# Kernel optimization log

Measured on AMD Instinct MI355X. Metric: run time of the kernel, lower is better.

## Reference

```python
import jax, jax.numpy as jnp
import numpy as np

EMBED_DIM = 1024
NUM_HEADS = 16
HEAD_DIM = EMBED_DIM // NUM_HEADS
EPS = 1e-6


def setup_inputs() -> dict:
    key = jax.random.key(0)
    ks = jax.random.split(key, 11)
    Lq, Lk, N = 4096, 4096, 4
    s = 1.0 / np.sqrt(EMBED_DIM)
    inp = {
        'q': jax.random.normal(ks[0], (Lq, N, EMBED_DIM), dtype=jnp.float32),
        'k': jax.random.normal(ks[1], (Lk, N, EMBED_DIM), dtype=jnp.float32),
        'v': jax.random.normal(ks[2], (Lk, N, EMBED_DIM), dtype=jnp.float32),
        'Wq': jax.random.normal(ks[3], (EMBED_DIM, EMBED_DIM), dtype=jnp.float32) * s,
        'bq': jax.random.normal(ks[4], (EMBED_DIM,), dtype=jnp.float32) * s,
        'Wk': jax.random.normal(ks[5], (EMBED_DIM, EMBED_DIM), dtype=jnp.float32) * s,
        'bk': jax.random.normal(ks[6], (EMBED_DIM,), dtype=jnp.float32) * s,
        'Wv': jax.random.normal(ks[7], (EMBED_DIM, EMBED_DIM), dtype=jnp.float32) * s,
        'bv': jax.random.normal(ks[8], (EMBED_DIM,), dtype=jnp.float32) * s,
        'Wo': jax.random.normal(ks[9], (EMBED_DIM, EMBED_DIM), dtype=jnp.float32) * s,
        'bo': jax.random.normal(ks[10], (EMBED_DIM,), dtype=jnp.float32) * s,
    }
    return inp


def _feature_map(x):
    # F.elu(x) + 1
    return jax.nn.elu(x) + 1.0


def reference(q, k, v, Wq, bq, Wk, bk, Wv, bv, Wo, bo):
    Lq, N, E = q.shape
    Lk = k.shape[0]
    # torch Linear: y = x @ W.T + b
    qp = q @ Wq.T + bq
    kp = k @ Wk.T + bk
    vp = v @ Wv.T + bv
    # (L, N, E) -> (N, H, L, D)
    qh = qp.reshape(Lq, N, NUM_HEADS, HEAD_DIM).transpose(1, 2, 0, 3)
    kh = kp.reshape(Lk, N, NUM_HEADS, HEAD_DIM).transpose(1, 2, 0, 3)
    vh = vp.reshape(Lk, N, NUM_HEADS, HEAD_DIM).transpose(1, 2, 0, 3)
    qf = _feature_map(qh)
    kf = _feature_map(kh)
    k_sum = kf.sum(axis=2)                               # (N, H, D)
    kv = jnp.einsum('nhld,nhle->nhde', kf, vh)            # (N, H, D, D)
    z = 1.0 / (jnp.einsum('nhld,nhd->nhl', qf, k_sum) + EPS)
    out = jnp.einsum('nhld,nhde->nhle', qf, kv) * z[..., None]
    out = out.transpose(2, 0, 1, 3).reshape(Lq, N, E)
    out = out @ Wo.T + bo
    return out
```

## Files before the change

kernel.cpp:

```cpp
#include <hip/hip_runtime.h>
#include <hip/hip_bf16.h>
#include <cstdint>


typedef __attribute__((ext_vector_type(8))) short bf16x8;
typedef __attribute__((ext_vector_type(4))) float f32x4;

#define L_SEQ 4096
#define NBATCH 4
#define EMB 1024
#define NHEADS 16
#define HDIM 64
#define MROWS (L_SEQ * NBATCH)
#define NHG (NBATCH * NHEADS)
#define LCHUNK 512
#define NCHUNK (L_SEQ / LCHUNK)

__device__ __forceinline__ unsigned short f2bf(float f) {
  union { float f; uint32_t u; } v; v.f = f;
  uint32_t u = v.u;
  u += 0x7fffu + ((u >> 16) & 1u);
  return (unsigned short)(u >> 16);
}
__device__ __forceinline__ float bf2f(unsigned short s) {
  union { uint32_t u; float f; } v; v.u = ((uint32_t)s) << 16;
  return v.f;
}
__device__ __forceinline__ uint32_t pkbf(float a, float b) {
  union { float f; uint32_t u; } ua, ub; ua.f = a; ub.f = b;
  return ((ua.u + 0x8000u) >> 16) | ((ub.u + 0x8000u) & 0xffff0000u);
}

__global__ __launch_bounds__(256) void convert_kernel(const float* __restrict__ src,
                                                      unsigned short* __restrict__ dst,
                                                      int n) {
  int i = (blockIdx.x * 256 + threadIdx.x) * 4;
  if (i + 4 <= n) {
    float4 f = *(const float4*)(src + i);
    uint2 p;
    p.x = pkbf(f.x, f.y);
    p.y = pkbf(f.z, f.w);
    *(uint2*)(dst + i) = p;
  }
}

__global__ __launch_bounds__(256) void convert_w4(const float* __restrict__ s0,
                                                  const float* __restrict__ s1,
                                                  const float* __restrict__ s2,
                                                  const float* __restrict__ s3,
                                                  unsigned short* __restrict__ d0,
                                                  unsigned short* __restrict__ d1,
                                                  unsigned short* __restrict__ d2,
                                                  unsigned short* __restrict__ d3,
                                                  int n) {
  const int w = blockIdx.y;
  const float* src = (w == 0) ? s0 : (w == 1) ? s1 : (w == 2) ? s2 : s3;
  unsigned short* dst = (w == 0) ? d0 : (w == 1) ? d1 : (w == 2) ? d2 : d3;
  int i = (blockIdx.x * 256 + threadIdx.x) * 4;
  if (i + 4 <= n) {
    float4 f = *(const float4*)(src + i);
    uint2 p;
    p.x = pkbf(f.x, f.y);
    p.y = pkbf(f.z, f.w);
    *(uint2*)(dst + i) = p;
  }
}


#define STAGE_H(MATB, RH, SLOT, KTN)                                            \
  do {                                                                          \
    _Pragma("unroll")                                                           \
    for (int r_ = 0; r_ < 2; r_++) {                                            \
      const long grow_ = ((MATB) ? bcol0 : arow0) + (RH) * 128 + r_ * 64 + srowt;\
      const unsigned short* gp_ =                                               \
          ((MATB) ? B : A) + grow_ * (long)K + (KTN) + skoff;                   \
      __builtin_amdgcn_global_load_lds(                                         \
          (const __attribute__((address_space(1))) void*)gp_,                   \
          (__attribute__((address_space(3))) void*)(smem + (MATB) * 65536 +     \
              (SLOT) * 16384 + r_ * 8192 + wid * 1024),                         \
          16, 0, 0);                                                            \
    }                                                                           \
  } while (0)

#define MFMA_Q(AF, BF, MFB, NFB)                                                \
  do {                                                                          \
    __builtin_amdgcn_s_setprio(1);                                              \
    _Pragma("unroll")                                                           \
    for (int mi_ = 0; mi_ < 4; mi_++)                                           \
      _Pragma("unroll")                                                         \
      for (int ni_ = 0; ni_ < 2; ni_++)                                         \
        _Pragma("unroll")                                                       \
        for (int ks_ = 0; ks_ < 2; ks_++)                                       \
          acc[(MFB) + mi_][(NFB) + ni_] =                                       \
              __builtin_amdgcn_mfma_f32_16x16x32_bf16(                          \
                  AF[mi_ * 2 + ks_], BF[ni_ * 2 + ks_],                         \
                  acc[(MFB) + mi_][(NFB) + ni_], 0, 0, 0);                      \
    __builtin_amdgcn_s_setprio(0);                                              \
  } while (0)

#define PH_SYNC                                                                 \
  __builtin_amdgcn_s_barrier();                                                 \
  asm volatile("s_waitcnt lgkmcnt(0)" ::: "memory");                            \
  __builtin_amdgcn_sched_barrier(0);

#define TILE_T(SA, K1, K2, S01, S23, VMODE)                                     \
  do {                                                                          \
    bf16x8 af0[8], af1[8], bf0[4], bf1[4];                                      \
             \
    _Pragma("unroll")                                                           \
    for (int mi_ = 0; mi_ < 4; mi_++)                                           \
      _Pragma("unroll")                                                         \
      for (int ks_ = 0; ks_ < 2; ks_++)                                         \
        af0[mi_ * 2 + ks_] = *(const bf16x8*)(smem + ((SA) + wr) * 16384 + aRB +\
                                              mi_ * 2048 + akt[ks_]);           \
    _Pragma("unroll")                                                           \
    for (int ni_ = 0; ni_ < 2; ni_++)                                           \
      _Pragma("unroll")                                                         \
      for (int ks_ = 0; ks_ < 2; ks_++)                                         \
        bf0[ni_ * 2 + ks_] = *(const bf16x8*)(smem + 65536 +                    \
                                              ((SA) + (wc >> 1)) * 16384 + bRB +\
                                              ni_ * 2048 + akt[ks_]);           \
    if (S01) STAGE_H(0, 1, (SA) ^ 3, K1);                                       \
    PH_SYNC                                                                     \
    MFMA_Q(af0, bf0, 0, 0);                                                     \
    __builtin_amdgcn_s_barrier();                                               \
                                      \
    _Pragma("unroll")                                                           \
    for (int ni_ = 0; ni_ < 2; ni_++)                                           \
      _Pragma("unroll")                                                         \
      for (int ks_ = 0; ks_ < 2; ks_++)                                         \
        bf1[ni_ * 2 + ks_] = *(const bf16x8*)(smem + 65536 +                    \
                                              ((SA) + (wc >> 1)) * 16384 + bRB +\
                                              (ni_ + 2) * 2048 + akt[ks_]);     \
    if (S01) STAGE_H(1, 1, (SA) ^ 3, K1);                                       \
    PH_SYNC                                                                     \
    MFMA_Q(af0, bf1, 0, 2);                                                     \
    __builtin_amdgcn_s_barrier();                                               \
                                  \
    _Pragma("unroll")                                                           \
    for (int mi_ = 0; mi_ < 4; mi_++)                                           \
      _Pragma("unroll")                                                         \
      for (int ks_ = 0; ks_ < 2; ks_++)                                         \
        af1[mi_ * 2 + ks_] = *(const bf16x8*)(smem + ((SA) + wr) * 16384 + aRB +\
                                              (mi_ + 4) * 2048 + akt[ks_]);     \
    if (S23) STAGE_H(1, 0, (SA), K2);                                           \
    PH_SYNC                                                                     \
    MFMA_Q(af1, bf1, 4, 2);                                                     \
    __builtin_amdgcn_s_barrier();                                               \
                     \
    if (S23) STAGE_H(0, 0, (SA), K2);                                           \
    PH_SYNC                                                                     \
    MFMA_Q(af1, bf0, 4, 0);                                                     \
    if ((VMODE) == 1) asm volatile("s_waitcnt vmcnt(4)" ::: "memory");          \
    if ((VMODE) == 2) asm volatile("s_waitcnt vmcnt(0)" ::: "memory");          \
    __builtin_amdgcn_s_barrier();                                               \
  } while (0)

template <int MODE>
__global__ __launch_bounds__(512, 2) void gemm_bt(const unsigned short* __restrict__ A,
                                                  const unsigned short* __restrict__ B,
                                                  const float* __restrict__ bias,
                                                  void* __restrict__ Cout,
                                                  int M, int Nn, int K) {
  __shared__ __align__(16) char smem[131072];

  const int tid   = threadIdx.x;
  const int wid   = tid >> 6;
  const int lane  = tid & 63;
  const int col16 = lane & 15;
  const int quad  = lane >> 4;
  const int wr = wid >> 2;
  const int wc = wid & 3;
  const long arow0 = (long)blockIdx.x * 256;
  const long bcol0 = (long)blockIdx.y * 256;

  const int axor = (col16 & 7) << 4;
  int akt[2];
  akt[0] = (quad * 16) ^ axor;
  akt[1] = (64 + quad * 16) ^ axor;
  const int aRB = col16 * 128;
  const int bRB = ((wc & 1) * 64 + col16) * 128;

  const int srowt = tid >> 3;
  const int skoff = (((tid & 7) * 16) ^ ((srowt & 7) << 4)) >> 1;

  const int NT = K >> 6;

  STAGE_H(0, 0, 0, 0);
  STAGE_H(0, 1, 1, 0);
  STAGE_H(1, 0, 0, 0);
  STAGE_H(1, 1, 1, 0);
  STAGE_H(1, 0, 2, 64);
  STAGE_H(0, 0, 2, 64);

  const f32x4 fzero = {0.f, 0.f, 0.f, 0.f};
  f32x4 acc[8][4];
#pragma unroll
  for (int i = 0; i < 8; i++)
#pragma unroll
    for (int j = 0; j < 4; j++) acc[i][j] = fzero;

  asm volatile("s_waitcnt vmcnt(4)" ::: "memory");
  __builtin_amdgcn_s_barrier();

#pragma unroll 1
  for (int u = 0; u + 4 <= NT; u += 2) {
    TILE_T(0, (u + 1) * 64, (u + 2) * 64, 1, 1, 1);
    TILE_T(2, (u + 2) * 64, (u + 3) * 64, 1, 1, 1);
  }
  TILE_T(0, (NT - 1) * 64, 0, 1, 0, 2);
  TILE_T(2, 0, 0, 0, 0, 0);

  float bcol[4];
#pragma unroll
  for (int nf = 0; nf < 4; nf++) bcol[nf] = bias[bcol0 + wc * 64 + nf * 16 + col16];

  const int erow = tid >> 4;
  const int ecc  = tid & 15;

  if (MODE != 2) {
    unsigned short* epi = (unsigned short*)smem;
    const int EST = 264;
#pragma unroll
    for (int s = 0; s < 8; s++) {
      if ((s >> 2) == wr) {
        const int mfb = (s & 3) * 2;
#pragma unroll
        for (int ml = 0; ml < 2; ml++)
#pragma unroll
          for (int nf = 0; nf < 4; nf++)
#pragma unroll
            for (int rr = 0; rr < 4; rr++) {
              float vv = acc[mfb + ml][nf][rr] + bcol[nf];
              if (MODE == 0) vv = (vv > 0.f) ? (vv + 1.f) : __expf(vv);
              epi[(ml * 16 + quad * 4 + rr) * EST + wc * 64 + nf * 16 + col16] =
                  f2bf(vv);
            }
      }
      __syncthreads();
      {
        const long gr = arow0 + s * 32 + erow;
        const unsigned short* srcp = &epi[erow * EST + ecc * 16];
        uint4 a  = *(const uint4*)srcp;
        uint4 b2 = *(const uint4*)(srcp + 8);
        unsigned short* Cp = (unsigned short*)Cout + gr * Nn + bcol0 + ecc * 16;
        *(uint4*)Cp       = a;
        *(uint4*)(Cp + 8) = b2;
      }
      __syncthreads();
    }
  } else {
    float* epi = (float*)smem;
    const int ESF = 260;
#pragma unroll
    for (int s = 0; s < 8; s++) {
      if ((s >> 2) == wr) {
        const int mfb = (s & 3) * 2;
#pragma unroll
        for (int ml = 0; ml < 2; ml++)
#pragma unroll
          for (int nf = 0; nf < 4; nf++)
#pragma unroll
            for (int rr = 0; rr < 4; rr++)
              epi[(ml * 16 + quad * 4 + rr) * ESF + wc * 64 + nf * 16 + col16] =
                  acc[mfb + ml][nf][rr] + bcol[nf];
      }
      __syncthreads();
      {
        const long gr = arow0 + s * 32 + erow;
        const float* srcp = &epi[erow * ESF + ecc * 16];
        float* Cp = (float*)Cout + gr * Nn + bcol0 + ecc * 16;
#pragma unroll
        for (int s4 = 0; s4 < 4; s4++)
          *(float4*)(Cp + s4 * 4) = *(const float4*)(srcp + s4 * 4);
      }
      __syncthreads();
    }
  }
}

__global__ __launch_bounds__(256) void kv_partial_kernel(const unsigned short* __restrict__ kf,
                                                         const unsigned short* __restrict__ vp,
                                                         float* __restrict__ kvp,
                                                         float* __restrict__ ksp) {
  __shared__ float ks[32 * 64];
  __shared__ float vs[32 * 64];
  const int hg = blockIdx.x;
  const int chunk = blockIdx.y;
  const int n = hg >> 4, h = hg & 15;
  const int tid = threadIdx.x;
  const int td = tid >> 4, te = tid & 15;
  const long hoff = (long)n * EMB + h * HDIM;
  const int l0 = chunk * LCHUNK;

  float acc[4][4];
#pragma unroll
  for (int i = 0; i < 4; i++)
#pragma unroll
    for (int j = 0; j < 4; j++) acc[i][j] = 0.f;
  float ksacc[4] = {0.f, 0.f, 0.f, 0.f};

  const int lrow = tid >> 3;
  const int dcol = (tid & 7) * 8;

  for (int ls = 0; ls < LCHUNK; ls += 32) {
    const long g = (long)(l0 + ls + lrow) * (NBATCH * EMB) + hoff + dcol;
    uint4 kr = *(const uint4*)(kf + g);
    uint4 vr = *(const uint4*)(vp + g);
    float* kd = &ks[lrow * 64 + dcol];
    float* vd = &vs[lrow * 64 + dcol];
    uint32_t ku[4] = {kr.x, kr.y, kr.z, kr.w};
    uint32_t vu[4] = {vr.x, vr.y, vr.z, vr.w};
#pragma unroll
    for (int t2 = 0; t2 < 4; t2++) {
      kd[2 * t2]     = bf2f((unsigned short)(ku[t2] & 0xffffu));
      kd[2 * t2 + 1] = bf2f((unsigned short)(ku[t2] >> 16));
      vd[2 * t2]     = bf2f((unsigned short)(vu[t2] & 0xffffu));
      vd[2 * t2 + 1] = bf2f((unsigned short)(vu[t2] >> 16));
    }
    __syncthreads();
#pragma unroll
    for (int l = 0; l < 32; l++) {
      float kq[4], vq[4];
      *(float4*)kq = *(const float4*)(&ks[l * 64 + td * 4]);
      *(float4*)vq = *(const float4*)(&vs[l * 64 + te * 4]);
#pragma unroll
      for (int i = 0; i < 4; i++) {
        ksacc[i] += kq[i];
#pragma unroll
        for (int j = 0; j < 4; j++) acc[i][j] += kq[i] * vq[j];
      }
    }
    __syncthreads();
  }
  float* outp = kvp + ((long)chunk * NHG + hg) * 4096;
#pragma unroll
  for (int i = 0; i < 4; i++)
#pragma unroll
    for (int j = 0; j < 4; j++)
      outp[(td * 4 + i) * 64 + te * 4 + j] = acc[i][j];
  if (te == 0) {
    float* o2 = ksp + ((long)chunk * NHG + hg) * 64;
#pragma unroll
    for (int i = 0; i < 4; i++) o2[td * 4 + i] = ksacc[i];
  }
}

__global__ __launch_bounds__(256) void attn_out_kernel(const unsigned short* __restrict__ qf,
                                                       const float* __restrict__ kvp,
                                                       const float* __restrict__ ksp,
                                                       unsigned short* __restrict__ out1) {
  __shared__ __align__(16) char smem[53248];
  const int hg = blockIdx.x;
  const int lc = blockIdx.y;
  const int n = hg >> 4, h = hg & 15;
  const int tid = threadIdx.x;
  const int wid = tid >> 6;
  const int lane = tid & 63;
  const int col16 = lane & 15;
  const int quad  = lane >> 4;
  const long lbase = (long)lc * 256;

#pragma unroll
  for (int r = 0; r < 8; r++) {
    const int row = r * 32 + (tid >> 3);
    const long l = lbase + row;
    const int sk = (((tid & 7) * 16) ^ ((row & 7) << 4)) >> 1;
    const unsigned short* gp = qf + (l * NBATCH + n) * (long)EMB + h * HDIM + sk;
    __builtin_amdgcn_global_load_lds(
        (const __attribute__((address_space(1))) void*)gp,
        (__attribute__((address_space(3))) void*)(smem + r * 4096 + tid * 16),
        16, 0, 0);
  }

  char* Bl = smem + 32768;
  for (int wb = tid * 4; wb < 4096; wb += 1024) {
    float4 s = make_float4(0.f, 0.f, 0.f, 0.f);
#pragma unroll
    for (int c = 0; c < NCHUNK; c++) {
      const float4 t = *(const float4*)(kvp + ((long)c * NHG + hg) * 4096 + wb);
      s.x += t.x; s.y += t.y; s.z += t.z; s.w += t.w;
    }
    const int d = wb >> 6;
    const int e0 = wb & 63;
    float sv[4] = {s.x, s.y, s.z, s.w};
#pragma unroll
    for (int j = 0; j < 4; j++) {
      const int e = e0 + j;
      const unsigned short hi = f2bf(sv[j]);
      const unsigned short lo = f2bf(sv[j] - bf2f(hi));
      const int key = (e & 7) << 4;
      *(unsigned short*)(Bl + e * 256 + ((2 * d) ^ key))       = hi;
      *(unsigned short*)(Bl + e * 256 + ((128 + 2 * d) ^ key)) = lo;
    }
  }
  if (tid < 64) {
    float s = 0.f;
#pragma unroll
    for (int c = 0; c < NCHUNK; c++) s += ksp[((long)c * NHG + hg) * 64 + tid];
    const unsigned short hi = f2bf(s);
    const unsigned short lo = f2bf(s - bf2f(hi));
    *(unsigned short*)(Bl + 64 * 256 + 2 * tid)       = hi;
    *(unsigned short*)(Bl + 64 * 256 + 128 + 2 * tid) = lo;
  }
  {
    uint32_t* zb = (uint32_t*)(Bl + 65 * 256);
    for (int i = tid; i < 15 * 64; i += 256) zb[i] = 0u;
  }
  __syncthreads();

  const int wl0 = wid * 64;
  const int akey = (col16 & 7) << 4;

  bf16x8 af[4][2];
#pragma unroll
  for (int mi = 0; mi < 4; mi++)
#pragma unroll
    for (int ks = 0; ks < 2; ks++)
      af[mi][ks] = *(const bf16x8*)(smem + (wl0 + mi * 16 + col16) * 128 +
                                    ((ks * 64 + quad * 16) ^ akey));

  const f32x4 fzero = {0.f, 0.f, 0.f, 0.f};
  f32x4 acc[4][5];
#pragma unroll
  for (int mi = 0; mi < 4; mi++)
#pragma unroll
    for (int nf = 0; nf < 5; nf++) acc[mi][nf] = fzero;

#pragma unroll
  for (int nf = 0; nf < 5; nf++) {
    bf16x8 bfr[4];
#pragma unroll
    for (int pass = 0; pass < 2; pass++)
#pragma unroll
      for (int ks = 0; ks < 2; ks++)
        bfr[pass * 2 + ks] = *(const bf16x8*)(Bl + (nf * 16 + col16) * 256 +
                                              ((pass * 128 + ks * 64 + quad * 16) ^ akey));
#pragma unroll
    for (int mi = 0; mi < 4; mi++)
#pragma unroll
      for (int pass = 0; pass < 2; pass++)
#pragma unroll
        for (int ks = 0; ks < 2; ks++)
          acc[mi][nf] = __builtin_amdgcn_mfma_f32_16x16x32_bf16(
              af[mi][ks], bfr[pass * 2 + ks], acc[mi][nf], 0, 0, 0);
  }

  __syncthreads();

  unsigned short* epi = (unsigned short*)smem;
#pragma unroll
  for (int mi = 0; mi < 4; mi++) {
#pragma unroll
    for (int rr = 0; rr < 4; rr++) {
      const float dv = __shfl(acc[mi][4][rr], lane & 48);
      const float z = 1.f / (dv + 1e-6f);
      const int row = wl0 + mi * 16 + quad * 4 + rr;
      const int key = (row & 7) << 4;
#pragma unroll
      for (int nf = 0; nf < 4; nf++)
        *(unsigned short*)((char*)epi + row * 128 +
                           (((nf * 16 + col16) * 2) ^ key)) =
            f2bf(acc[mi][nf][rr] * z);
    }
  }
  __syncthreads();

#pragma unroll
  for (int r = 0; r < 8; r++) {
    const int row = r * 32 + (tid >> 3);
    const long l = lbase + row;
    const uint4 vv = *(const uint4*)((char*)epi + row * 128 +
                                     (((tid & 7) * 16) ^ ((row & 7) << 4)));
    *(uint4*)(out1 + (l * NBATCH + n) * (long)EMB + h * HDIM + (tid & 7) * 8) = vv;
  }
}

extern "C" void kernel_launch(void* const* d_in, const int* in_sizes, int n_in,
                              void* d_out, int out_size, void* d_ws, size_t ws_size,
                              hipStream_t stream) {
  const float* q  = (const float*)d_in[0];
  const float* k  = (const float*)d_in[1];
  const float* v  = (const float*)d_in[2];
  const float* Wq = (const float*)d_in[3];
  const float* bq = (const float*)d_in[4];
  const float* Wk = (const float*)d_in[5];
  const float* bk = (const float*)d_in[6];
  const float* Wv = (const float*)d_in[7];
  const float* bv = (const float*)d_in[8];
  const float* Wo = (const float*)d_in[9];
  const float* bo = (const float*)d_in[10];

  char* ws = (char*)d_ws;
  const size_t BUF = (size_t)MROWS * EMB * 2;
  unsigned short* T0  = (unsigned short*)(ws);
  unsigned short* qf  = (unsigned short*)(ws + BUF);
  unsigned short* kf  = (unsigned short*)(ws + 2 * BUF);
  unsigned short* vp  = (unsigned short*)(ws + 3 * BUF);
  unsigned short* Wqb = (unsigned short*)(ws + 4 * BUF);
  unsigned short* Wkb = Wqb + (size_t)EMB * EMB;
  unsigned short* Wvb = Wkb + (size_t)EMB * EMB;
  unsigned short* Wob = Wvb + (size_t)EMB * EMB;
  float* kvp = (float*)(ws + 4 * BUF + 4 * (size_t)EMB * EMB * 2);
  float* ksp = kvp + (size_t)NCHUNK * NHG * HDIM * HDIM;

  const int nQKV = MROWS * EMB;
  const int nW   = EMB * EMB;

  convert_w4<<<dim3(nW / 1024, 4), 256, 0, stream>>>(Wq, Wk, Wv, Wo,
                                                     Wqb, Wkb, Wvb, Wob, nW);

  dim3 gg(MROWS / 256, EMB / 256), bb(512);

  convert_kernel<<<nQKV / 1024, 256, 0, stream>>>(q, T0, nQKV);
  gemm_bt<0><<<gg, bb, 0, stream>>>(T0, Wqb, bq, qf, MROWS, EMB, EMB);
  convert_kernel<<<nQKV / 1024, 256, 0, stream>>>(k, T0, nQKV);
  gemm_bt<0><<<gg, bb, 0, stream>>>(T0, Wkb, bk, kf, MROWS, EMB, EMB);
  convert_kernel<<<nQKV / 1024, 256, 0, stream>>>(v, T0, nQKV);
  gemm_bt<1><<<gg, bb, 0, stream>>>(T0, Wvb, bv, vp, MROWS, EMB, EMB);

  kv_partial_kernel<<<dim3(NHG, NCHUNK), 256, 0, stream>>>(kf, vp, kvp, ksp);
  attn_out_kernel<<<dim3(NHG, L_SEQ / 256), 256, 0, stream>>>(qf, kvp, ksp, T0);

  gemm_bt<2><<<gg, bb, 0, stream>>>(T0, Wob, bo, d_out, MROWS, EMB, EMB);
}
```

Before: 453.3 us.

## Batch QKV projections into one launch and hoist KV reduction into its own kernel

Converts q, k and v to bf16 in a single three-way launch and runs all three projection GEMMs as one grid with a z-dimension selecting the operands. This fills the device with three times as many blocks and removes launch gaps between the serial per-projection steps. The per-chunk KV partial sums are now reduced and packed into the swizzled bf16 hi/lo layout once per head by a new kernel. Previously every attention block redid that reduction; it now loads the packed result straight into LDS. The batched path needs extra workspace for separate k/v buffers and falls back to the old sequence when the workspace is too small.

```diff
diff --git a/kernel.cpp b/kernel.cpp
--- a/kernel.cpp
+++ b/kernel.cpp
@@ -15,6 +15,7 @@
 #define NHG (NBATCH * NHEADS)
 #define LCHUNK 512
 #define NCHUNK (L_SEQ / LCHUNK)
+#define KVB_SH 10240
 
 __device__ __forceinline__ unsigned short f2bf(float f) {
   union { float f; uint32_t u; } v; v.f = f;
@@ -34,6 +35,26 @@
 __global__ __launch_bounds__(256) void convert_kernel(const float* __restrict__ src,
                                                       unsigned short* __restrict__ dst,
                                                       int n) {
+  int i = (blockIdx.x * 256 + threadIdx.x) * 4;
+  if (i + 4 <= n) {
+    float4 f = *(const float4*)(src + i);
+    uint2 p;
+    p.x = pkbf(f.x, f.y);
+    p.y = pkbf(f.z, f.w);
+    *(uint2*)(dst + i) = p;
+  }
+}
+
+__global__ __launch_bounds__(256) void convert_x3(const float* __restrict__ s0,
+                                                  const float* __restrict__ s1,
+                                                  const float* __restrict__ s2,
+                                                  unsigned short* __restrict__ d0,
+                                                  unsigned short* __restrict__ d1,
+                                                  unsigned short* __restrict__ d2,
+                                                  int n) {
+  const int w = blockIdx.y;
+  const float* src = (w == 0) ? s0 : (w == 1) ? s1 : s2;
+  unsigned short* dst = (w == 0) ? d0 : (w == 1) ? d1 : d2;
   int i = (blockIdx.x * 256 + threadIdx.x) * 4;
   if (i + 4 <= n) {
     float4 f = *(const float4*)(src + i);
@@ -156,14 +177,13 @@
     __builtin_amdgcn_s_barrier();                                               \
   } while (0)
 
-template <int MODE>
-__global__ __launch_bounds__(512, 2) void gemm_bt(const unsigned short* __restrict__ A,
-                                                  const unsigned short* __restrict__ B,
-                                                  const float* __restrict__ bias,
-                                                  void* __restrict__ Cout,
-                                                  int M, int Nn, int K) {
-  __shared__ __align__(16) char smem[131072];
-
+template <int OUTF32>
+__device__ __forceinline__ void gemm_body(char* smem,
+                                          const unsigned short* __restrict__ A,
+                                          const unsigned short* __restrict__ B,
+                                          const float* __restrict__ bias,
+                                          void* __restrict__ Cout,
+                                          int M, int Nn, int K, bool act) {
   const int tid   = threadIdx.x;
   const int wid   = tid >> 6;
   const int lane  = tid & 63;
@@ -218,7 +238,7 @@
   const int erow = tid >> 4;
   const int ecc  = tid & 15;
 
-  if (MODE != 2) {
+  if constexpr (OUTF32 == 0) {
     unsigned short* epi = (unsigned short*)smem;
     const int EST = 264;
 #pragma unroll
@@ -232,7 +252,7 @@
 #pragma unroll
             for (int rr = 0; rr < 4; rr++) {
               float vv = acc[mfb + ml][nf][rr] + bcol[nf];
-              if (MODE == 0) vv = (vv > 0.f) ? (vv + 1.f) : __expf(vv);
+              if (act) vv = (vv > 0.f) ? (vv + 1.f) : __expf(vv);
               epi[(ml * 16 + quad * 4 + rr) * EST + wc * 64 + nf * 16 + col16] =
                   f2bf(vv);
             }
@@ -279,6 +299,35 @@
   }
 }
 
+template <int MODE>
+__global__ __launch_bounds__(512, 2) void gemm_bt(const unsigned short* __restrict__ A,
+                                                  const unsigned short* __restrict__ B,
+                                                  const float* __restrict__ bias,
+                                                  void* __restrict__ Cout,
+                                                  int M, int Nn, int K) {
+  __shared__ __align__(16) char smem[131072];
+  gemm_body<(MODE == 2) ? 1 : 0>(smem, A, B, bias, Cout, M, Nn, K, MODE == 0);
+}
+
+__global__ __launch_bounds__(512, 2) void gemm_bt3(
+    const unsigned short* __restrict__ A0, const unsigned short* __restrict__ A1,
+    const unsigned short* __restrict__ A2,
+    const unsigned short* __restrict__ B0, const unsigned short* __restrict__ B1,
+    const unsigned short* __restrict__ B2,
+    const float* __restrict__ b0, const float* __restrict__ b1,
+    const float* __restrict__ b2,
+    unsigned short* __restrict__ C0, unsigned short* __restrict__ C1,
+    unsigned short* __restrict__ C2,
+    int M, int Nn, int K) {
+  __shared__ __align__(16) char smem[131072];
+  const int z = blockIdx.z;
+  const unsigned short* A = (z == 0) ? A0 : (z == 1) ? A1 : A2;
+  const unsigned short* B = (z == 0) ? B0 : (z == 1) ? B1 : B2;
+  const float* bias       = (z == 0) ? b0 : (z == 1) ? b1 : b2;
+  unsigned short* C       = (z == 0) ? C0 : (z == 1) ? C1 : C2;
+  gemm_body<0>(smem, A, B, bias, C, M, Nn, K, z < 2);
+}
+
 __global__ __launch_bounds__(256) void kv_partial_kernel(const unsigned short* __restrict__ kf,
                                                          const unsigned short* __restrict__ vp,
                                                          float* __restrict__ kvp,
@@ -346,9 +395,50 @@
   }
 }
 
+__global__ __launch_bounds__(256) void kv_reduce(const float* __restrict__ kvp,
+                                                 const float* __restrict__ ksp,
+                                                 unsigned short* __restrict__ kvB) {
+  const int hg = blockIdx.x;
+  const int tid = threadIdx.x;
+  unsigned short* gB = kvB + (long)hg * KVB_SH;
+
+  for (int wb = tid * 4; wb < 4096; wb += 1024) {
+    float4 s = make_float4(0.f, 0.f, 0.f, 0.f);
+#pragma unroll
+    for (int c = 0; c < NCHUNK; c++) {
+      const float4 t = *(const float4*)(kvp + ((long)c * NHG + hg) * 4096 + wb);
+      s.x += t.x; s.y += t.y; s.z += t.z; s.w += t.w;
+    }
+    const int d = wb >> 6;
+    const int e0 = wb & 63;
+    float sv[4] = {s.x, s.y, s.z, s.w};
+#pragma unroll
+    for (int j = 0; j < 4; j++) {
+      const int e = e0 + j;
+      const unsigned short hi = f2bf(sv[j]);
+      const unsigned short lo = f2bf(sv[j] - bf2f(hi));
+      const int key = (e & 7) << 4;
+      gB[(e * 256 + ((2 * d) ^ key)) >> 1]       = hi;
+      gB[(e * 256 + ((128 + 2 * d) ^ key)) >> 1] = lo;
+    }
+  }
+  if (tid < 64) {
+    float s = 0.f;
+#pragma unroll
+    for (int c = 0; c < NCHUNK; c++) s += ksp[((long)c * NHG + hg) * 64 + tid];
+    const unsigned short hi = f2bf(s);
+    const unsigned short lo = f2bf(s - bf2f(hi));
+    gB[(64 * 256 + 2 * tid) >> 1]       = hi;
+    gB[(64 * 256 + 128 + 2 * tid) >> 1] = lo;
+  }
+  {
+    uint32_t* zb = (uint32_t*)(gB + 65 * 128);
+    for (int i = tid; i < 15 * 64; i += 256) zb[i] = 0u;
+  }
+}
+
 __global__ __launch_bounds__(256) void attn_out_kernel(const unsigned short* __restrict__ qf,
-                                                       const float* __restrict__ kvp,
-                                                       const float* __restrict__ ksp,
+                                                       const unsigned short* __restrict__ kvB,
                                                        unsigned short* __restrict__ out1) {
   __shared__ __align__(16) char smem[53248];
   const int hg = blockIdx.x;
@@ -372,43 +462,19 @@
         (__attribute__((address_space(3))) void*)(smem + r * 4096 + tid * 16),
         16, 0, 0);
   }
+  {
+    const unsigned short* gB = kvB + (long)hg * KVB_SH;
+#pragma unroll
+    for (int r = 0; r < 5; r++) {
+      __builtin_amdgcn_global_load_lds(
+          (const __attribute__((address_space(1))) void*)(gB + r * 2048 + tid * 8),
+          (__attribute__((address_space(3))) void*)(smem + 32768 + r * 4096 + tid * 16),
+          16, 0, 0);
+    }
+  }
+  __syncthreads();
 
   char* Bl = smem + 32768;
-  for (int wb = tid * 4; wb < 4096; wb += 1024) {
-    float4 s = make_float4(0.f, 0.f, 0.f, 0.f);
-#pragma unroll
-    for (int c = 0; c < NCHUNK; c++) {
-      const float4 t = *(const float4*)(kvp + ((long)c * NHG + hg) * 4096 + wb);
-      s.x += t.x; s.y += t.y; s.z += t.z; s.w += t.w;
-    }
-    const int d = wb >> 6;
-    const int e0 = wb & 63;
-    float sv[4] = {s.x, s.y, s.z, s.w};
-#pragma unroll
-    for (int j = 0; j < 4; j++) {
-      const int e = e0 + j;
-      const unsigned short hi = f2bf(sv[j]);
-      const unsigned short lo = f2bf(sv[j] - bf2f(hi));
-      const int key = (e & 7) << 4;
-      *(unsigned short*)(Bl + e * 256 + ((2 * d) ^ key))       = hi;
-      *(unsigned short*)(Bl + e * 256 + ((128 + 2 * d) ^ key)) = lo;
-    }
-  }
-  if (tid < 64) {
-    float s = 0.f;
-#pragma unroll
-    for (int c = 0; c < NCHUNK; c++) s += ksp[((long)c * NHG + hg) * 64 + tid];
-    const unsigned short hi = f2bf(s);
-    const unsigned short lo = f2bf(s - bf2f(hi));
-    *(unsigned short*)(Bl + 64 * 256 + 2 * tid)       = hi;
-    *(unsigned short*)(Bl + 64 * 256 + 128 + 2 * tid) = lo;
-  }
-  {
-    uint32_t* zb = (uint32_t*)(Bl + 65 * 256);
-    for (int i = tid; i < 15 * 64; i += 256) zb[i] = 0u;
-  }
-  __syncthreads();
-
   const int wl0 = wid * 64;
   const int akey = (col16 & 7) << 4;
 
@@ -492,35 +558,72 @@
   const float* bo = (const float*)d_in[10];
 
   char* ws = (char*)d_ws;
-  const size_t BUF = (size_t)MROWS * EMB * 2;
-  unsigned short* T0  = (unsigned short*)(ws);
-  unsigned short* qf  = (unsigned short*)(ws + BUF);
-  unsigned short* kf  = (unsigned short*)(ws + 2 * BUF);
-  unsigned short* vp  = (unsigned short*)(ws + 3 * BUF);
-  unsigned short* Wqb = (unsigned short*)(ws + 4 * BUF);
-  unsigned short* Wkb = Wqb + (size_t)EMB * EMB;
-  unsigned short* Wvb = Wkb + (size_t)EMB * EMB;
-  unsigned short* Wob = Wvb + (size_t)EMB * EMB;
-  float* kvp = (float*)(ws + 4 * BUF + 4 * (size_t)EMB * EMB * 2);
-  float* ksp = kvp + (size_t)NCHUNK * NHG * HDIM * HDIM;
+  const size_t BUF  = (size_t)MROWS * EMB * 2;
+  const size_t WSZ  = 4 * (size_t)EMB * EMB * 2;
+  const size_t KVPZ = (size_t)NCHUNK * NHG * 4096 * 4;
+  const size_t KSPZ = (size_t)NCHUNK * NHG * 64 * 4;
+  const size_t KVBZ = (size_t)NHG * KVB_SH * 2;
 
   const int nQKV = MROWS * EMB;
   const int nW   = EMB * EMB;
-
-  convert_w4<<<dim3(nW / 1024, 4), 256, 0, stream>>>(Wq, Wk, Wv, Wo,
-                                                     Wqb, Wkb, Wvb, Wob, nW);
-
   dim3 gg(MROWS / 256, EMB / 256), bb(512);
 
-  convert_kernel<<<nQKV / 1024, 256, 0, stream>>>(q, T0, nQKV);
-  gemm_bt<0><<<gg, bb, 0, stream>>>(T0, Wqb, bq, qf, MROWS, EMB, EMB);
-  convert_kernel<<<nQKV / 1024, 256, 0, stream>>>(k, T0, nQKV);
-  gemm_bt<0><<<gg, bb, 0, stream>>>(T0, Wkb, bk, kf, MROWS, EMB, EMB);
-  convert_kernel<<<nQKV / 1024, 256, 0, stream>>>(v, T0, nQKV);
-  gemm_bt<1><<<gg, bb, 0, stream>>>(T0, Wvb, bv, vp, MROWS, EMB, EMB);
-
-  kv_partial_kernel<<<dim3(NHG, NCHUNK), 256, 0, stream>>>(kf, vp, kvp, ksp);
-  attn_out_kernel<<<dim3(NHG, L_SEQ / 256), 256, 0, stream>>>(qf, kvp, ksp, T0);
-
-  gemm_bt<2><<<gg, bb, 0, stream>>>(T0, Wob, bo, d_out, MROWS, EMB, EMB);
-}
+  const size_t need_batched = 6 * BUF + WSZ + KVPZ + KSPZ + KVBZ;
+
+  if (ws_size >= need_batched) {
+    unsigned short* T0  = (unsigned short*)(ws);
+    unsigned short* kb  = (unsigned short*)(ws + BUF);
+    unsigned short* vb  = (unsigned short*)(ws + 2 * BUF);
+    unsigned short* qf  = (unsigned short*)(ws + 3 * BUF);
+    unsigned short* kf  = (unsigned short*)(ws + 4 * BUF);
+    unsigned short* vp  = (unsigned short*)(ws + 5 * BUF);
+    unsigned short* Wqb = (unsigned short*)(ws + 6 * BUF);
+    unsigned short* Wkb = Wqb + (size_t)EMB * EMB;
+    unsigned short* Wvb = Wkb + (size_t)EMB * EMB;
+    unsigned short* Wob = Wvb + (size_t)EMB * EMB;
+    float* kvp = (float*)(ws + 6 * BUF + WSZ);
+    float* ksp = (float*)(ws + 6 * BUF + WSZ + KVPZ);
+    unsigned short* kvB = (unsigned short*)(ws + 6 * BUF + WSZ + KVPZ + KSPZ);
+
+    convert_w4<<<dim3(nW / 1024, 4), 256, 0, stream>>>(Wq, Wk, Wv, Wo,
+                                                       Wqb, Wkb, Wvb, Wob, nW);
+    convert_x3<<<dim3(nQKV / 1024, 3), 256, 0, stream>>>(q, k, v, T0, kb, vb, nQKV);
+
+    gemm_bt3<<<dim3(MROWS / 256, EMB / 256, 3), bb, 0, stream>>>(
+        T0, kb, vb, Wqb, Wkb, Wvb, bq, bk, bv, qf, kf, vp, MROWS, EMB, EMB);
+
+    kv_partial_kernel<<<dim3(NHG, NCHUNK), 256, 0, stream>>>(kf, vp, kvp, ksp);
+    kv_reduce<<<NHG, 256, 0, stream>>>(kvp, ksp, kvB);
+    attn_out_kernel<<<dim3(NHG, L_SEQ / 256), 256, 0, stream>>>(qf, kvB, T0);
+
+    gemm_bt<2><<<gg, bb, 0, stream>>>(T0, Wob, bo, d_out, MROWS, EMB, EMB);
+  } else {
+    unsigned short* T0  = (unsigned short*)(ws);
+    unsigned short* qf  = (unsigned short*)(ws + BUF);
+    unsigned short* kf  = (unsigned short*)(ws + 2 * BUF);
+    unsigned short* vp  = (unsigned short*)(ws + 3 * BUF);
+    unsigned short* Wqb = (unsigned short*)(ws + 4 * BUF);
+    unsigned short* Wkb = Wqb + (size_t)EMB * EMB;
+    unsigned short* Wvb = Wkb + (size_t)EMB * EMB;
+    unsigned short* Wob = Wvb + (size_t)EMB * EMB;
+    float* kvp = (float*)(ws + 4 * BUF + WSZ);
+    float* ksp = (float*)(ws + 4 * BUF + WSZ + KVPZ);
+    unsigned short* kvB = (unsigned short*)(ws + 4 * BUF + WSZ + KVPZ + KSPZ);
+
+    convert_w4<<<dim3(nW / 1024, 4), 256, 0, stream>>>(Wq, Wk, Wv, Wo,
+                                                       Wqb, Wkb, Wvb, Wob, nW);
+
+    convert_kernel<<<nQKV / 1024, 256, 0, stream>>>(q, T0, nQKV);
+    gemm_bt<0><<<gg, bb, 0, stream>>>(T0, Wqb, bq, qf, MROWS, EMB, EMB);
+    convert_kernel<<<nQKV / 1024, 256, 0, stream>>>(k, T0, nQKV);
+    gemm_bt<0><<<gg, bb, 0, stream>>>(T0, Wkb, bk, kf, MROWS, EMB, EMB);
+    convert_kernel<<<nQKV / 1024, 256, 0, stream>>>(v, T0, nQKV);
+    gemm_bt<1><<<gg, bb, 0, stream>>>(T0, Wvb, bv, vp, MROWS, EMB, EMB);
+
+    kv_partial_kernel<<<dim3(NHG, NCHUNK), 256, 0, stream>>>(kf, vp, kvp, ksp);
+    kv_reduce<<<NHG, 256, 0, stream>>>(kvp, ksp, kvB);
+    attn_out_kernel<<<dim3(NHG, L_SEQ / 256), 256, 0, stream>>>(qf, kvB, T0);
+
+    gemm_bt<2><<<gg, bb, 0, stream>>>(T0, Wob, bo, d_out, MROWS, EMB, EMB);
+  }
+}
```

Result: slower. 463.0 us (+2.1%).

## Compute per-chunk KV outer products with bf16 MFMA and fold k_sum in

Applied to the files above, without the earlier changes.

Replaces the scalar fp32 outer-product loop in kv_partial_kernel with bf16 MFMA 16x16x32 instructions. K and V tiles are staged transposed in LDS as bf16 with padded rows. An extra block of V rows holding ones (first row 1.0, rest zero) makes one MFMA tile produce the k_sum column, so no separate reduction is needed. This removes the per-element bf16-to-fp32 conversion and the scalar FMAs, at the cost of transposing stores into LDS that may cause bank conflicts.

```diff
diff --git a/kernel.cpp b/kernel.cpp
--- a/kernel.cpp
+++ b/kernel.cpp
@@ -15,6 +15,7 @@
 #define NHG (NBATCH * NHEADS)
 #define LCHUNK 512
 #define NCHUNK (L_SEQ / LCHUNK)
+#define KTS 72
 
 __device__ __forceinline__ unsigned short f2bf(float f) {
   union { float f; uint32_t u; } v; v.f = f;
@@ -283,66 +284,73 @@
                                                          const unsigned short* __restrict__ vp,
                                                          float* __restrict__ kvp,
                                                          float* __restrict__ ksp) {
-  __shared__ float ks[32 * 64];
-  __shared__ float vs[32 * 64];
+  __shared__ __align__(16) unsigned short ks_t[64 * KTS];
+  __shared__ __align__(16) unsigned short vs_t[80 * KTS];
   const int hg = blockIdx.x;
   const int chunk = blockIdx.y;
   const int n = hg >> 4, h = hg & 15;
   const int tid = threadIdx.x;
-  const int td = tid >> 4, te = tid & 15;
+  const int wid = tid >> 6;
+  const int lane = tid & 63;
+  const int col16 = lane & 15;
+  const int quad  = lane >> 4;
   const long hoff = (long)n * EMB + h * HDIM;
   const int l0 = chunk * LCHUNK;
 
-  float acc[4][4];
-#pragma unroll
-  for (int i = 0; i < 4; i++)
-#pragma unroll
-    for (int j = 0; j < 4; j++) acc[i][j] = 0.f;
-  float ksacc[4] = {0.f, 0.f, 0.f, 0.f};
-
-  const int lrow = tid >> 3;
-  const int dcol = (tid & 7) * 8;
-
-  for (int ls = 0; ls < LCHUNK; ls += 32) {
-    const long g = (long)(l0 + ls + lrow) * (NBATCH * EMB) + hoff + dcol;
-    uint4 kr = *(const uint4*)(kf + g);
-    uint4 vr = *(const uint4*)(vp + g);
-    float* kd = &ks[lrow * 64 + dcol];
-    float* vd = &vs[lrow * 64 + dcol];
-    uint32_t ku[4] = {kr.x, kr.y, kr.z, kr.w};
-    uint32_t vu[4] = {vr.x, vr.y, vr.z, vr.w};
-#pragma unroll
-    for (int t2 = 0; t2 < 4; t2++) {
-      kd[2 * t2]     = bf2f((unsigned short)(ku[t2] & 0xffffu));
-      kd[2 * t2 + 1] = bf2f((unsigned short)(ku[t2] >> 16));
-      vd[2 * t2]     = bf2f((unsigned short)(vu[t2] & 0xffffu));
-      vd[2 * t2 + 1] = bf2f((unsigned short)(vu[t2] >> 16));
-    }
+  const int sl  = tid >> 2;
+  const int sd0 = (tid & 3) * 16;
+
+  for (int i = tid; i < 16 * KTS; i += 256)
+    vs_t[64 * KTS + i] = (i < KTS) ? (unsigned short)0x3F80u : (unsigned short)0u;
+
+  const f32x4 fzero = {0.f, 0.f, 0.f, 0.f};
+  f32x4 acc[5];
+#pragma unroll
+  for (int nf = 0; nf < 5; nf++) acc[nf] = fzero;
+
+  for (int ls = 0; ls < LCHUNK; ls += 64) {
+    const long g = (long)(l0 + ls + sl) * (NBATCH * EMB) + hoff + sd0;
+    uint4 kr0 = *(const uint4*)(kf + g);
+    uint4 kr1 = *(const uint4*)(kf + g + 8);
+    uint4 vr0 = *(const uint4*)(vp + g);
+    uint4 vr1 = *(const uint4*)(vp + g + 8);
     __syncthreads();
-#pragma unroll
-    for (int l = 0; l < 32; l++) {
-      float kq[4], vq[4];
-      *(float4*)kq = *(const float4*)(&ks[l * 64 + td * 4]);
-      *(float4*)vq = *(const float4*)(&vs[l * 64 + te * 4]);
-#pragma unroll
-      for (int i = 0; i < 4; i++) {
-        ksacc[i] += kq[i];
-#pragma unroll
-        for (int j = 0; j < 4; j++) acc[i][j] += kq[i] * vq[j];
+    {
+      uint32_t ku[8] = {kr0.x, kr0.y, kr0.z, kr0.w, kr1.x, kr1.y, kr1.z, kr1.w};
+      uint32_t vu[8] = {vr0.x, vr0.y, vr0.z, vr0.w, vr1.x, vr1.y, vr1.z, vr1.w};
+#pragma unroll
+      for (int t = 0; t < 8; t++) {
+        ks_t[(sd0 + 2 * t)     * KTS + sl] = (unsigned short)(ku[t] & 0xffffu);
+        ks_t[(sd0 + 2 * t + 1) * KTS + sl] = (unsigned short)(ku[t] >> 16);
+        vs_t[(sd0 + 2 * t)     * KTS + sl] = (unsigned short)(vu[t] & 0xffffu);
+        vs_t[(sd0 + 2 * t + 1) * KTS + sl] = (unsigned short)(vu[t] >> 16);
       }
     }
     __syncthreads();
-  }
+#pragma unroll
+    for (int kk = 0; kk < 2; kk++) {
+      const bf16x8 af =
+          *(const bf16x8*)(&ks_t[(wid * 16 + col16) * KTS + kk * 32 + quad * 8]);
+#pragma unroll
+      for (int nf = 0; nf < 5; nf++) {
+        const bf16x8 bfv =
+            *(const bf16x8*)(&vs_t[(nf * 16 + col16) * KTS + kk * 32 + quad * 8]);
+        acc[nf] = __builtin_amdgcn_mfma_f32_16x16x32_bf16(af, bfv, acc[nf], 0, 0, 0);
+      }
+    }
+  }
+
   float* outp = kvp + ((long)chunk * NHG + hg) * 4096;
-#pragma unroll
-  for (int i = 0; i < 4; i++)
-#pragma unroll
-    for (int j = 0; j < 4; j++)
-      outp[(td * 4 + i) * 64 + te * 4 + j] = acc[i][j];
-  if (te == 0) {
+  const int dr = wid * 16 + quad * 4;
+#pragma unroll
+  for (int nf = 0; nf < 4; nf++)
+#pragma unroll
+    for (int rr = 0; rr < 4; rr++)
+      outp[(dr + rr) * 64 + nf * 16 + col16] = acc[nf][rr];
+  if (col16 == 0) {
     float* o2 = ksp + ((long)chunk * NHG + hg) * 64;
 #pragma unroll
-    for (int i = 0; i < 4; i++) o2[td * 4 + i] = ksacc[i];
+    for (int rr = 0; rr < 4; rr++) o2[dr + rr] = acc[4][rr];
   }
 }
 
```

After: 437.5 us. -3.5%, faster.
